# Kernel tuning notes

Measured on AMD Instinct MI355X. Metric: run time of the kernel, lower is better.

## Reference

```python
import jax, jax.numpy as jnp
import numpy as np

N = 50000      # nodes
E = 800000     # edges (avg degree 16)
D_IN, D_H, D_OUT = 128, 96, 32


def _lin(x, W, b):
    return x @ W.T + b


def _transformer_conv(x, src, dst, Wq, bq, Wk, bk, Wv, bv, Ws, bs, n):
    # PyG TransformerConv, heads=1: q_i . k_j / sqrt(d), segment softmax over
    # incoming edges of each target node, weighted sum of values, plus skip.
    q = _lin(x, Wq, bq)            # [N, d]
    k = _lin(x, Wk, bk)            # [N, d]
    v = _lin(x, Wv, bv)            # [N, d]
    d = q.shape[-1]
    score = jnp.sum(q[dst] * k[src], axis=-1) / jnp.sqrt(jnp.float32(d))  # [E]
    m = jax.ops.segment_max(score, dst, num_segments=n)                   # [N]
    m = jnp.where(jnp.isneginf(m), 0.0, m)   # isolated nodes
    e = jnp.exp(score - m[dst])                                           # [E]
    denom = jax.ops.segment_sum(e, dst, num_segments=n)                   # [N]
    alpha = e / jnp.maximum(denom[dst], 1e-16)                            # [E]
    agg = jax.ops.segment_sum(alpha[:, None] * v[src], dst, num_segments=n)
    return agg + _lin(x, Ws, bs)   # root weight (skip connection)


def setup_inputs() -> dict:
    key = jax.random.key(0)
    ks = jax.random.split(key, 32)
    x = jax.random.normal(ks[0], (N, D_IN), dtype=jnp.float32)
    edge_index = jax.random.randint(ks[1], (2, E), 0, N, dtype=jnp.int64)
    dims = [(D_IN, D_H), (D_H, D_H), (D_H, D_OUT)]
    inp = {"x": x, "edge_index": edge_index}
    ki = 2
    for li, (fi, fo) in enumerate(dims, start=1):
        s = 1.0 / np.sqrt(fi)
        for nm in ("Wq", "Wk", "Wv", "Ws"):
            inp[f"{nm}{li}"] = jax.random.normal(ks[ki], (fo, fi), dtype=jnp.float32) * s
            ki += 1
        for nm in ("bq", "bk", "bv", "bs"):
            inp[f"{nm}{li}"] = jnp.zeros((fo,), dtype=jnp.float32)
    return inp


def reference(x, edge_index,
              Wq1, Wk1, Wv1, Ws1, bq1, bk1, bv1, bs1,
              Wq2, Wk2, Wv2, Ws2, bq2, bk2, bv2, bs2,
              Wq3, Wk3, Wv3, Ws3, bq3, bk3, bv3, bs3):
    src, dst = edge_index[0], edge_index[1]
    h = jax.nn.relu(_transformer_conv(x, src, dst, Wq1, bq1, Wk1, bk1, Wv1, bv1, Ws1, bs1, N))
    h = jax.nn.relu(_transformer_conv(h, src, dst, Wq2, bq2, Wk2, bk2, Wv2, bv2, Ws2, bs2, N))
    h = _transformer_conv(h, src, dst, Wq3, bq3, Wk3, bk3, Wv3, bv3, Ws3, bs3, N)
    return jax.nn.log_softmax(h, axis=1)
```

## Files before the change

kernel.cpp:

```cpp
#include <hip/hip_runtime.h>
#include <math.h>

typedef __attribute__((ext_vector_type(8))) __bf16 bf16x8;
typedef __attribute__((ext_vector_type(8))) short short8;
typedef __attribute__((ext_vector_type(4))) float f32x4;
typedef unsigned int uint;
typedef unsigned short ushort;
typedef unsigned char uchar;


__device__ inline bf16x8 ld_bf8(const ushort* p){
  short8 s = *reinterpret_cast<const short8*>(p);
  return __builtin_bit_cast(bf16x8, s);
}

__device__ inline ushort f2bf(float f){
  return __builtin_bit_cast(ushort, (__bf16)f);
}
__device__ inline uint pack2bf(float a, float b){
  return (uint)f2bf(a) | ((uint)f2bf(b) << 16);
}
__device__ inline float bf_lo(uint u){ return __builtin_bit_cast(float, u << 16); }
__device__ inline float bf_hi(uint u){ return __builtin_bit_cast(float, u & 0xFFFF0000u); }

template<int S>
__device__ inline float unp8(uint w){
  return __builtin_amdgcn_cvt_f32_fp8((int)w, S);
}
__device__ inline uint pk8(float a, float b, float c, float d){
  int r = 0;
  r = __builtin_amdgcn_cvt_pk_fp8_f32(a, b, r, false);
  r = __builtin_amdgcn_cvt_pk_fp8_f32(c, d, r, true);
  return (uint)r;
}


__global__ __launch_bounds__(256) void k_bucketA(const int* __restrict__ dst,
                                                 int* __restrict__ gbh, int E){
  __shared__ int cnt[256];
  cnt[threadIdx.x] = 0;
  __syncthreads();
  for (int e = blockIdx.x * blockDim.x + threadIdx.x; e < E; e += gridDim.x * blockDim.x)
    atomicAdd(&cnt[dst[e] >> 8], 1);
  __syncthreads();
  int c = cnt[threadIdx.x];
  if (c > 0) atomicAdd(&gbh[threadIdx.x], c);
}

__global__ __launch_bounds__(256) void k_bscan(const int* __restrict__ gbh,
                                               int* __restrict__ gbase,
                                               int* __restrict__ gcur, int NB, int E){
  __shared__ int wsum[4];
  int t = threadIdx.x;
  int c = (t < NB) ? gbh[t] : 0;
  int lane = t & 63, wv = t >> 6;
  int incl = c;
  #pragma unroll
  for (int o = 1; o < 64; o <<= 1){
    int x = __shfl_up(incl, o);
    if (lane >= o) incl += x;
  }
  if (lane == 63) wsum[wv] = incl;
  __syncthreads();
  int woff = 0;
  for (int w = 0; w < wv; ++w) woff += wsum[w];
  int excl = woff + incl - c;
  if (t < NB){ gbase[t] = excl; gcur[t] = excl; }
  if (t == 0) gbase[NB] = E;
}

#define CS_CHUNK 4096
__global__ __launch_bounds__(256) void k_bucketB(const int* __restrict__ src,
                                                 const int* __restrict__ dst,
                                                 int* __restrict__ gcur,
                                                 uint* __restrict__ epack, int E){
  __shared__ int cnt[256];
  __shared__ int wcur[256];
  const int b0 = blockIdx.x * CS_CHUNK;
  const int b1 = (b0 + CS_CHUNK < E) ? b0 + CS_CHUNK : E;
  cnt[threadIdx.x] = 0;
  __syncthreads();
  for (int e = b0 + threadIdx.x; e < b1; e += 256)
    atomicAdd(&cnt[dst[e] >> 8], 1);
  __syncthreads();
  int c = cnt[threadIdx.x];
  int base = (c > 0) ? atomicAdd(&gcur[threadIdx.x], c) : 0;
  wcur[threadIdx.x] = base;
  __syncthreads();
  for (int e = b0 + threadIdx.x; e < b1; e += 256){
    int d = dst[e];
    int s = src[e];
    int pos = atomicAdd(&wcur[d >> 8], 1);
    epack[pos] = ((uint)d << 16) | (uint)(s & 0xFFFF);
  }
}

__global__ __launch_bounds__(256) void k_bucketC(const uint* __restrict__ epack,
                                                 const int* __restrict__ gbase,
                                                 int* __restrict__ offs,
                                                 ushort* __restrict__ srclist,
                                                 int N, int E){
  __shared__ int cnt[256];
  __shared__ int wcur[256];
  __shared__ int wsum[4];
  const int b = blockIdx.x;
  const int lo = gbase[b], hi = gbase[b + 1];
  cnt[threadIdx.x] = 0;
  __syncthreads();
  for (int i = lo + threadIdx.x; i < hi; i += 256)
    atomicAdd(&cnt[(epack[i] >> 16) & 255], 1);
  __syncthreads();
  int c = cnt[threadIdx.x];
  int lane = threadIdx.x & 63, wv = threadIdx.x >> 6;
  int incl = c;
  #pragma unroll
  for (int o = 1; o < 64; o <<= 1){
    int x = __shfl_up(incl, o);
    if (lane >= o) incl += x;
  }
  if (lane == 63) wsum[wv] = incl;
  __syncthreads();
  int woff = 0;
  for (int w = 0; w < wv; ++w) woff += wsum[w];
  int excl = lo + woff + incl - c;
  int d = (b << 8) + threadIdx.x;
  if (d < N) offs[d] = excl;
  wcur[threadIdx.x] = excl;
  __syncthreads();
  for (int i = lo + threadIdx.x; i < hi; i += 256){
    uint ep = epack[i];
    int pos = atomicAdd(&wcur[(ep >> 16) & 255], 1);
    srclist[pos] = (ushort)(ep & 0xFFFF);
  }
  if (b == 0 && threadIdx.x == 0) offs[N] = E;
}


struct WSet { const float* src[12]; ushort* dst[12]; int n[12]; };

__global__ __launch_bounds__(256) void k_castw(WSet ws, int* __restrict__ gbh){
  int m = blockIdx.y;
  if (m == 12){
    if (blockIdx.x == 0) gbh[threadIdx.x] = 0;
    return;
  }
  int n = ws.n[m];
  const float* s = ws.src[m];
  ushort* d = ws.dst[m];
  for (int i = blockIdx.x * blockDim.x + threadIdx.x; i < n; i += gridDim.x * blockDim.x)
    d[i] = f2bf(s[i]);
}


template<int KT, int NT, bool F32IN>
__global__ __launch_bounds__(256) void k_proj(
    const ushort* __restrict__ hin, const float* __restrict__ hinf, int N,
    const ushort* __restrict__ Wq, const ushort* __restrict__ Wk,
    const ushort* __restrict__ Wv, const ushort* __restrict__ Wsk,
    const float* __restrict__ bq, const float* __restrict__ bk,
    const float* __restrict__ bv, const float* __restrict__ bs,
    ushort* __restrict__ qo, uchar* __restrict__ kv8,
    ushort* __restrict__ so, int kvstB)
{
  constexpr int K  = KT * 32;
  constexpr int PS = K + 16;
  constexpr int FO = NT * 16;
  __shared__ ushort alds[32 * PS];

  const int row0 = blockIdx.x * 32;

  for (int idx = threadIdx.x; idx < 32 * (K / 8); idx += 256){
    int r  = idx / (K / 8);
    int c8 = idx - r * (K / 8);
    int rr = row0 + r; if (rr >= N) rr = N - 1;
    if constexpr (F32IN){
      const float* xr = hinf + (size_t)rr * K + c8 * 8;
      float4 a = reinterpret_cast<const float4*>(xr)[0];
      float4 c = reinterpret_cast<const float4*>(xr)[1];
      uint4 u;
      u.x = pack2bf(a.x, a.y); u.y = pack2bf(a.z, a.w);
      u.z = pack2bf(c.x, c.y); u.w = pack2bf(c.z, c.w);
      *reinterpret_cast<uint4*>(&alds[r * PS + c8 * 8]) = u;
    } else {
      *reinterpret_cast<short8*>(&alds[r * PS + c8 * 8]) =
          *reinterpret_cast<const short8*>(hin + (size_t)rr * K + c8 * 8);
    }
  }
  __syncthreads();

  const int mat  = threadIdx.x >> 6;
  const int lane = threadIdx.x & 63;
  const int r16  = lane & 15;
  const int kg   = lane >> 4;

  const ushort* W = (mat == 0) ? Wq : (mat == 1) ? Wk : (mat == 2) ? Wv : Wsk;
  const float*  b = (mat == 0) ? bq : (mat == 1) ? bk : (mat == 2) ? bv : bs;

  bf16x8 af[2][KT];
  #pragma unroll
  for (int m = 0; m < 2; ++m)
    #pragma unroll
    for (int kt = 0; kt < KT; ++kt)
      af[m][kt] = ld_bf8(&alds[(m * 16 + r16) * PS + kt * 32 + kg * 8]);

  f32x4 acc[2][NT];
  #pragma unroll
  for (int nt = 0; nt < NT; ++nt){
    float4 bb = *reinterpret_cast<const float4*>(b + nt * 16 + kg * 4);
    #pragma unroll
    for (int m = 0; m < 2; ++m){
      acc[m][nt][0] = bb.x; acc[m][nt][1] = bb.y;
      acc[m][nt][2] = bb.z; acc[m][nt][3] = bb.w;
    }
  }

  #pragma unroll
  for (int nt = 0; nt < NT; ++nt){
    bf16x8 wf[KT];
    #pragma unroll
    for (int kt = 0; kt < KT; ++kt)
      wf[kt] = ld_bf8(W + (size_t)(nt * 16 + r16) * K + kt * 32 + kg * 8);
    #pragma unroll
    for (int kt = 0; kt < KT; ++kt){
      acc[0][nt] = __builtin_amdgcn_mfma_f32_16x16x32_bf16(wf[kt], af[0][kt], acc[0][nt], 0, 0, 0);
      acc[1][nt] = __builtin_amdgcn_mfma_f32_16x16x32_bf16(wf[kt], af[1][kt], acc[1][nt], 0, 0, 0);
    }
  }

  #pragma unroll
  for (int m = 0; m < 2; ++m){
    const int row = row0 + m * 16 + r16;
    if (row < N){
      if (mat == 0 || mat == 3){
        ushort* out = (mat == 0) ? qo : so;
        #pragma unroll
        for (int nt = 0; nt < NT; ++nt){
          uint* p = reinterpret_cast<uint*>(out + (size_t)row * FO + nt * 16 + kg * 4);
          p[0] = pack2bf(acc[m][nt][0], acc[m][nt][1]);
          p[1] = pack2bf(acc[m][nt][2], acc[m][nt][3]);
        }
      } else {
        const int voff = (mat == 2) ? FO : 0;
        #pragma unroll
        for (int nt = 0; nt < NT; ++nt){
          uint u = pk8(acc[m][nt][0], acc[m][nt][1], acc[m][nt][2], acc[m][nt][3]);
          *reinterpret_cast<uint*>(kv8 + (size_t)row * kvstB + voff + nt * 16 + kg * 4) = u;
        }
      }
    }
  }
}


template<int FO, int MODE>
__global__ __launch_bounds__(256) void k_attn3(
    const ushort* __restrict__ qb, const uchar* __restrict__ kv,
    const ushort* __restrict__ skipb, const int* __restrict__ offs,
    const ushort* __restrict__ srclist, void* __restrict__ outp,
    int N, float scale)
{
  constexpr int G   = 8;
  constexpr int FPL = FO / G;
  constexpr int KW  = FPL / 4;
  constexpr int KVB = 2 * FO;
  const int lane = threadIdx.x & 63;
  const int sub  = lane & 7;
  const int node = (blockIdx.x * (blockDim.x >> 6) + (threadIdx.x >> 6)) * 8 + (lane >> 3);
  const bool nv  = node < N;
  const int nodec = nv ? node : 0;

  const uint2* qrow = reinterpret_cast<const uint2*>(qb + (size_t)nodec * FO + sub * FPL);
  float qf[FPL];
  #pragma unroll
  for (int w = 0; w < KW; ++w){
    uint2 t = qrow[w];
    qf[4 * w]     = bf_lo(t.x); qf[4 * w + 1] = bf_hi(t.x);
    qf[4 * w + 2] = bf_lo(t.y); qf[4 * w + 3] = bf_hi(t.y);
  }

  float m = -INFINITY, l = 0.f;
  float acc[FPL];
  #pragma unroll
  for (int f = 0; f < FPL; ++f) acc[f] = 0.f;

  const int e0 = nv ? offs[node] : 0;
  const int e1 = nv ? offs[node + 1] : 0;

  uint kA[4][KW], vA[4][KW], kB[4][KW], vB[4][KW];

  auto DOLOAD = [&](int eb, uint (*Kr)[KW], uint (*Vr)[KW]){
    #pragma unroll
    for (int i = 0; i < 4; ++i){
      int ee = eb + i;
      int ec = (ee < e1) ? ee : (e1 - 1);
      int j = srclist[ec];
      const uchar* row = kv + (size_t)j * KVB;
      const uint* rk = reinterpret_cast<const uint*>(row + sub * FPL);
      const uint* rv = reinterpret_cast<const uint*>(row + FO + sub * FPL);
      #pragma unroll
      for (int w = 0; w < KW; ++w){
        Kr[i][w] = rk[w];
        Vr[i][w] = rv[w];
      }
    }
  };

  auto COMPUTE = [&](uint (*Kr)[KW], uint (*Vr)[KW], int ebase){
    float s[4];
    #pragma unroll
    for (int i = 0; i < 4; ++i){
      float t = 0.f;
      #pragma unroll
      for (int w = 0; w < KW; ++w){
        uint kwd = Kr[i][w];
        t = fmaf(qf[4 * w],     unp8<0>(kwd), t);
        t = fmaf(qf[4 * w + 1], unp8<1>(kwd), t);
        t = fmaf(qf[4 * w + 2], unp8<2>(kwd), t);
        t = fmaf(qf[4 * w + 3], unp8<3>(kwd), t);
      }
      s[i] = t;
    }
    #pragma unroll
    for (int o = 1; o < G; o <<= 1){
      s[0] += __shfl_xor(s[0], o);
      s[1] += __shfl_xor(s[1], o);
      s[2] += __shfl_xor(s[2], o);
      s[3] += __shfl_xor(s[3], o);
    }
    s[0] = s[0] * scale;
    s[1] = (ebase + 1 < e1) ? s[1] * scale : -1e30f;
    s[2] = (ebase + 2 < e1) ? s[2] * scale : -1e30f;
    s[3] = (ebase + 3 < e1) ? s[3] * scale : -1e30f;

    float mnew = fmaxf(fmaxf(m, s[0]), fmaxf(fmaxf(s[1], s[2]), s[3]));
    float sfac = __expf(m - mnew);
    float p4[4];
    p4[0] = __expf(s[0] - mnew);
    p4[1] = __expf(s[1] - mnew);
    p4[2] = __expf(s[2] - mnew);
    p4[3] = __expf(s[3] - mnew);
    l = l * sfac + (p4[0] + p4[1]) + (p4[2] + p4[3]);
    #pragma unroll
    for (int f = 0; f < FPL; ++f) acc[f] *= sfac;
    #pragma unroll
    for (int i = 0; i < 4; ++i){
      #pragma unroll
      for (int w = 0; w < KW; ++w){
        uint vwd = Vr[i][w];
        acc[4 * w]     = fmaf(p4[i], unp8<0>(vwd), acc[4 * w]);
        acc[4 * w + 1] = fmaf(p4[i], unp8<1>(vwd), acc[4 * w + 1]);
        acc[4 * w + 2] = fmaf(p4[i], unp8<2>(vwd), acc[4 * w + 2]);
        acc[4 * w + 3] = fmaf(p4[i], unp8<3>(vwd), acc[4 * w + 3]);
      }
    }
    m = mnew;
  };

  if (e0 < e1){
    int e = e0;
    DOLOAD(e, kA, vA);
    for (;;){
      int en = e + 4;
      bool more = en < e1;
      if (more) DOLOAD(en, kB, vB);
      COMPUTE(kA, vA, e);
      e = en;
      if (!more) break;
      en = e + 4;
      more = en < e1;
      if (more) DOLOAD(en, kA, vA);
      COMPUTE(kB, vB, e);
      e = en;
      if (!more) break;
    }
  }

  float inv = 1.f / fmaxf(l, 1e-16f);
  const uint2* srow = reinterpret_cast<const uint2*>(skipb + (size_t)nodec * FO + sub * FPL);
  float val[FPL];
  #pragma unroll
  for (int w = 0; w < KW; ++w){
    uint2 t = srow[w];
    val[4 * w]     = bf_lo(t.x) + acc[4 * w] * inv;
    val[4 * w + 1] = bf_hi(t.x) + acc[4 * w + 1] * inv;
    val[4 * w + 2] = bf_lo(t.y) + acc[4 * w + 2] * inv;
    val[4 * w + 3] = bf_hi(t.y) + acc[4 * w + 3] * inv;
  }

  if (MODE == 0){
    if (nv){
      uint2* orow = reinterpret_cast<uint2*>((ushort*)outp + (size_t)node * FO + sub * FPL);
      #pragma unroll
      for (int w = 0; w < KW; ++w){
        uint2 o;
        o.x = pack2bf(fmaxf(val[4 * w], 0.f),     fmaxf(val[4 * w + 1], 0.f));
        o.y = pack2bf(fmaxf(val[4 * w + 2], 0.f), fmaxf(val[4 * w + 3], 0.f));
        orow[w] = o;
      }
    }
  } else {
    float mx = -INFINITY;
    #pragma unroll
    for (int f = 0; f < FPL; ++f) mx = fmaxf(mx, val[f]);
    #pragma unroll
    for (int o = 1; o < G; o <<= 1) mx = fmaxf(mx, __shfl_xor(mx, o));
    float ssum = 0.f;
    #pragma unroll
    for (int f = 0; f < FPL; ++f) ssum += __expf(val[f] - mx);
    #pragma unroll
    for (int o = 1; o < G; o <<= 1) ssum += __shfl_xor(ssum, o);
    float lg = __logf(ssum);
    if (nv){
      float* orow = (float*)outp + (size_t)node * FO + sub * FPL;
      #pragma unroll
      for (int f = 0; f < FPL; ++f) orow[f] = val[f] - mx - lg;
    }
  }
}


extern "C" void kernel_launch(void* const* d_in, const int* in_sizes, int n_in,
                              void* d_out, int out_size, void* d_ws, size_t ws_size,
                              hipStream_t stream)
{
  const float* x  = (const float*)d_in[0];
  const int*   ei = (const int*)d_in[1];
  const int N = in_sizes[0] / 128;
  const int E = in_sizes[1] / 2;

  const float* W1[4]; const float* b1[4];
  const float* W2[4]; const float* b2[4];
  const float* W3[4]; const float* b3[4];
  for (int i = 0; i < 4; ++i){
    W1[i] = (const float*)d_in[2 + i];   b1[i] = (const float*)d_in[6 + i];
    W2[i] = (const float*)d_in[10 + i];  b2[i] = (const float*)d_in[14 + i];
    W3[i] = (const float*)d_in[18 + i];  b3[i] = (const float*)d_in[22 + i];
  }

  size_t off = 0;
  auto alloc = [&](size_t bytes) -> void* {
    void* p = (char*)d_ws + off;
    off = (off + bytes + 255) & ~(size_t)255;
    return p;
  };
  const int NB = (N + 255) / 256;
  int* offs       = (int*)alloc(((size_t)N + 1) * 4);
  int* gbh        = (int*)alloc(256 * 4);
  int* gbase      = (int*)alloc(260 * 4);
  int* gcur       = (int*)alloc(256 * 4);
  uint* epack     = (uint*)alloc((size_t)E * 4);
  ushort* srclist = (ushort*)alloc((size_t)E * 2);
  ushort* qb  = (ushort*)alloc((size_t)N * 96 * 2);
  uchar*  kvb = (uchar*)alloc((size_t)N * 192);
  ushort* sb  = (ushort*)alloc((size_t)N * 96 * 2);
  ushort* hb  = (ushort*)alloc((size_t)N * 128 * 2);
  ushort* wb  = (ushort*)alloc((size_t)98304 * 2);

  ushort* Wb1[4]; ushort* Wb2[4]; ushort* Wb3[4];
  for (int i = 0; i < 4; ++i){
    Wb1[i] = wb + (size_t)i * 12288;
    Wb2[i] = wb + 49152 + (size_t)i * 9216;
    Wb3[i] = wb + 49152 + 36864 + (size_t)i * 3072;
  }

  WSet wset;
  for (int i = 0; i < 4; ++i){
    wset.src[i]     = W1[i]; wset.dst[i]     = Wb1[i]; wset.n[i]     = 12288;
    wset.src[4 + i] = W2[i]; wset.dst[4 + i] = Wb2[i]; wset.n[4 + i] = 9216;
    wset.src[8 + i] = W3[i]; wset.dst[8 + i] = Wb3[i]; wset.n[8 + i] = 3072;
  }
  k_castw<<<dim3(48, 13), dim3(256), 0, stream>>>(wset, gbh);

  const int* esrc = ei;
  const int* edst = ei + E;
  k_bucketA<<<dim3(392), dim3(256), 0, stream>>>(edst, gbh, E);
  k_bscan<<<dim3(1), dim3(256), 0, stream>>>(gbh, gbase, gcur, NB, E);
  const int nCB = (E + CS_CHUNK - 1) / CS_CHUNK;
  k_bucketB<<<dim3(nCB), dim3(256), 0, stream>>>(esrc, edst, gcur, epack, E);
  k_bucketC<<<dim3(NB), dim3(256), 0, stream>>>(epack, gbase, offs, srclist, N, E);

  float* outf = (float*)d_out;
  const float sc96 = 1.0f / sqrtf(96.f);
  const float sc32 = 1.0f / sqrtf(32.f);

  const int gridP = (N + 31) / 32;
  const int gridA = (N + 31) / 32;

  k_proj<4, 6, true><<<dim3(gridP), dim3(256), 0, stream>>>(nullptr, x, N,
      Wb1[0], Wb1[1], Wb1[2], Wb1[3], b1[0], b1[1], b1[2], b1[3],
      qb, kvb, sb, 192);
  k_attn3<96, 0><<<dim3(gridA), dim3(256), 0, stream>>>(qb, kvb, sb, offs, srclist, hb, N, sc96);

  k_proj<3, 6, false><<<dim3(gridP), dim3(256), 0, stream>>>(hb, nullptr, N,
      Wb2[0], Wb2[1], Wb2[2], Wb2[3], b2[0], b2[1], b2[2], b2[3],
      qb, kvb, sb, 192);
  k_attn3<96, 0><<<dim3(gridA), dim3(256), 0, stream>>>(qb, kvb, sb, offs, srclist, hb, N, sc96);

  k_proj<3, 2, false><<<dim3(gridP), dim3(256), 0, stream>>>(hb, nullptr, N,
      Wb3[0], Wb3[1], Wb3[2], Wb3[3], b3[0], b3[1], b3[2], b3[3],
      qb, kvb, sb, 64);
  k_attn3<32, 1><<<dim3(gridA), dim3(256), 0, stream>>>(qb, kvb, sb, offs, srclist, outf, N, sc32);
}
```

Measured before the change: 193.4 us.

## Sort nodes by in-degree and schedule attention over degree-ordered permutation

Counts node in-degrees (clamped to 63) during CSR construction, scans the histogram and builds a permutation grouping nodes of equal degree. All three attention kernels read their node through this permutation so the 8 nodes sharing a wavefront have similar edge counts, reducing lane idling from degree imbalance. It adds two small kernels with heavily contended global atomics, and makes q/skip reads and output writes scattered rather than contiguous.

```diff
diff --git a/kernel.cpp b/kernel.cpp
--- a/kernel.cpp
+++ b/kernel.cpp
@@ -99,6 +99,7 @@
                                                  const int* __restrict__ gbase,
                                                  int* __restrict__ offs,
                                                  ushort* __restrict__ srclist,
+                                                 int* __restrict__ dcnt,
                                                  int N, int E){
   __shared__ int cnt[256];
   __shared__ int wcur[256];
@@ -124,7 +125,11 @@
   for (int w = 0; w < wv; ++w) woff += wsum[w];
   int excl = lo + woff + incl - c;
   int d = (b << 8) + threadIdx.x;
-  if (d < N) offs[d] = excl;
+  if (d < N){
+    offs[d] = excl;
+    int dg = c; if (dg > 63) dg = 63;
+    atomicAdd(&dcnt[dg], 1);
+  }
   wcur[threadIdx.x] = excl;
   __syncthreads();
   for (int i = lo + threadIdx.x; i < hi; i += 256){
@@ -135,13 +140,41 @@
   if (b == 0 && threadIdx.x == 0) offs[N] = E;
 }
 
+__global__ __launch_bounds__(64) void k_dscan(const int* __restrict__ dcnt,
+                                              int* __restrict__ dcur){
+  int lane = threadIdx.x;
+  int c = dcnt[lane];
+  int incl = c;
+  #pragma unroll
+  for (int o = 1; o < 64; o <<= 1){
+    int x = __shfl_up(incl, o);
+    if (lane >= o) incl += x;
+  }
+  dcur[lane] = incl - c;
+}
+
+__global__ __launch_bounds__(256) void k_dfill(const int* __restrict__ offs,
+                                               int* __restrict__ dcur,
+                                               int* __restrict__ perm, int N){
+  for (int n = blockIdx.x * blockDim.x + threadIdx.x; n < N; n += gridDim.x * blockDim.x){
+    int dg = offs[n + 1] - offs[n];
+    if (dg > 63) dg = 63;
+    int pos = atomicAdd(&dcur[dg], 1);
+    perm[pos] = n;
+  }
+}
+
 
 struct WSet { const float* src[12]; ushort* dst[12]; int n[12]; };
 
-__global__ __launch_bounds__(256) void k_castw(WSet ws, int* __restrict__ gbh){
+__global__ __launch_bounds__(256) void k_castw(WSet ws, int* __restrict__ gbh,
+                                               int* __restrict__ dcnt){
   int m = blockIdx.y;
   if (m == 12){
-    if (blockIdx.x == 0) gbh[threadIdx.x] = 0;
+    if (blockIdx.x == 0){
+      gbh[threadIdx.x] = 0;
+      if (threadIdx.x < 64) dcnt[threadIdx.x] = 0;
+    }
     return;
   }
   int n = ws.n[m];
@@ -256,8 +289,8 @@
 __global__ __launch_bounds__(256) void k_attn3(
     const ushort* __restrict__ qb, const uchar* __restrict__ kv,
     const ushort* __restrict__ skipb, const int* __restrict__ offs,
-    const ushort* __restrict__ srclist, void* __restrict__ outp,
-    int N, float scale)
+    const ushort* __restrict__ srclist, const int* __restrict__ perm,
+    void* __restrict__ outp, int N, float scale)
 {
   constexpr int G   = 8;
   constexpr int FPL = FO / G;
@@ -265,11 +298,11 @@
   constexpr int KVB = 2 * FO;
   const int lane = threadIdx.x & 63;
   const int sub  = lane & 7;
-  const int node = (blockIdx.x * (blockDim.x >> 6) + (threadIdx.x >> 6)) * 8 + (lane >> 3);
-  const bool nv  = node < N;
-  const int nodec = nv ? node : 0;
-
-  const uint2* qrow = reinterpret_cast<const uint2*>(qb + (size_t)nodec * FO + sub * FPL);
+  const int slot = (blockIdx.x * (blockDim.x >> 6) + (threadIdx.x >> 6)) * 8 + (lane >> 3);
+  const bool nv  = slot < N;
+  const int node = nv ? perm[slot] : 0;
+
+  const uint2* qrow = reinterpret_cast<const uint2*>(qb + (size_t)node * FO + sub * FPL);
   float qf[FPL];
   #pragma unroll
   for (int w = 0; w < KW; ++w){
@@ -376,7 +409,7 @@
   }
 
   float inv = 1.f / fmaxf(l, 1e-16f);
-  const uint2* srow = reinterpret_cast<const uint2*>(skipb + (size_t)nodec * FO + sub * FPL);
+  const uint2* srow = reinterpret_cast<const uint2*>(skipb + (size_t)node * FO + sub * FPL);
   float val[FPL];
   #pragma unroll
   for (int w = 0; w < KW; ++w){
@@ -448,6 +481,9 @@
   int* gbh        = (int*)alloc(256 * 4);
   int* gbase      = (int*)alloc(260 * 4);
   int* gcur       = (int*)alloc(256 * 4);
+  int* dcnt       = (int*)alloc(64 * 4);
+  int* dcur       = (int*)alloc(64 * 4);
+  int* perm       = (int*)alloc((size_t)N * 4);
   uint* epack     = (uint*)alloc((size_t)E * 4);
   ushort* srclist = (ushort*)alloc((size_t)E * 2);
   ushort* qb  = (ushort*)alloc((size_t)N * 96 * 2);
@@ -469,7 +505,7 @@
     wset.src[4 + i] = W2[i]; wset.dst[4 + i] = Wb2[i]; wset.n[4 + i] = 9216;
     wset.src[8 + i] = W3[i]; wset.dst[8 + i] = Wb3[i]; wset.n[8 + i] = 3072;
   }
-  k_castw<<<dim3(48, 13), dim3(256), 0, stream>>>(wset, gbh);
+  k_castw<<<dim3(48, 13), dim3(256), 0, stream>>>(wset, gbh, dcnt);
 
   const int* esrc = ei;
   const int* edst = ei + E;
@@ -477,7 +513,9 @@
   k_bscan<<<dim3(1), dim3(256), 0, stream>>>(gbh, gbase, gcur, NB, E);
   const int nCB = (E + CS_CHUNK - 1) / CS_CHUNK;
   k_bucketB<<<dim3(nCB), dim3(256), 0, stream>>>(esrc, edst, gcur, epack, E);
-  k_bucketC<<<dim3(NB), dim3(256), 0, stream>>>(epack, gbase, offs, srclist, N, E);
+  k_bucketC<<<dim3(NB), dim3(256), 0, stream>>>(epack, gbase, offs, srclist, dcnt, N, E);
+  k_dscan<<<dim3(1), dim3(64), 0, stream>>>(dcnt, dcur);
+  k_dfill<<<dim3(98), dim3(256), 0, stream>>>(offs, dcur, perm, N);
 
   float* outf = (float*)d_out;
   const float sc96 = 1.0f / sqrtf(96.f);
@@ -489,15 +527,15 @@
   k_proj<4, 6, true><<<dim3(gridP), dim3(256), 0, stream>>>(nullptr, x, N,
       Wb1[0], Wb1[1], Wb1[2], Wb1[3], b1[0], b1[1], b1[2], b1[3],
       qb, kvb, sb, 192);
-  k_attn3<96, 0><<<dim3(gridA), dim3(256), 0, stream>>>(qb, kvb, sb, offs, srclist, hb, N, sc96);
+  k_attn3<96, 0><<<dim3(gridA), dim3(256), 0, stream>>>(qb, kvb, sb, offs, srclist, perm, hb, N, sc96);
 
   k_proj<3, 6, false><<<dim3(gridP), dim3(256), 0, stream>>>(hb, nullptr, N,
       Wb2[0], Wb2[1], Wb2[2], Wb2[3], b2[0], b2[1], b2[2], b2[3],
       qb, kvb, sb, 192);
-  k_attn3<96, 0><<<dim3(gridA), dim3(256), 0, stream>>>(qb, kvb, sb, offs, srclist, hb, N, sc96);
+  k_attn3<96, 0><<<dim3(gridA), dim3(256), 0, stream>>>(qb, kvb, sb, offs, srclist, perm, hb, N, sc96);
 
   k_proj<3, 2, false><<<dim3(gridP), dim3(256), 0, stream>>>(hb, nullptr, N,
       Wb3[0], Wb3[1], Wb3[2], Wb3[3], b3[0], b3[1], b3[2], b3[3],
       qb, kvb, sb, 64);
-  k_attn3<32, 1><<<dim3(gridA), dim3(256), 0, stream>>>(qb, kvb, sb, offs, srclist, outf, N, sc32);
-}
+  k_attn3<32, 1><<<dim3(gridA), dim3(256), 0, stream>>>(qb, kvb, sb, offs, srclist, perm, outf, N, sc32);
+}
```

Measured after the change: 458.7 us. +137.2%, slower.
